# Optimization experiments

Measured on AMD Instinct MI355X. Metric: run time of the kernel, lower is better.

The kernel has to match this reference:

```python
import jax, jax.numpy as jnp
import numpy as np

# Tier config (cumulative d_model [256,1024,2048], cumulative heads [4,12,24], d_k=64)
TIER_OWN = [256, 768, 1024]      # per-tier own hidden dims
HEAD_OUT = [256, 512, 768]       # n_heads_per_tier[i] * d_k
NHS = [4, 8, 12]
DKS = [64, 64, 64]
RANK = 8
IN_OFF = np.cumsum([0] + TIER_OWN)    # [0,256,1024,2048]
OUT_OFF = np.cumsum([0] + HEAD_OUT)   # [0,256,768,1536]


def _block_ut_weight(key, in_dims, out_dims):
    """Full (sum_in, sum_out) matrix with lower-triangular blocks zeroed."""
    io = np.cumsum([0] + list(in_dims))
    oo = np.cumsum([0] + list(out_dims))
    n = len(in_dims)
    mask = np.zeros((io[-1], oo[-1]), dtype=np.float32)
    for i in range(n):
        for j in range(i, n):
            mask[io[i]:io[i + 1], oo[j]:oo[j + 1]] = 1.0
    W = jax.random.normal(key, (io[-1], oo[-1]), dtype=jnp.float32) * 0.02
    return W * jnp.asarray(mask)


def setup_inputs() -> dict:
    key = jax.random.key(0)
    ks = jax.random.split(key, 16)
    B, T, D = 4, 1024, 2048
    x = jax.random.normal(ks[0], (B, T, D), dtype=jnp.float32)
    W_Q = _block_ut_weight(ks[1], TIER_OWN, HEAD_OUT)
    W_K = _block_ut_weight(ks[2], TIER_OWN, HEAD_OUT)
    W_V = _block_ut_weight(ks[3], TIER_OWN, HEAD_OUT)
    W_O = _block_ut_weight(ks[4], HEAD_OUT, TIER_OWN)
    # feedback for tiers 0 and 1 (tier 2 has no higher tiers)
    hi0 = TIER_OWN[1] + TIER_OWN[2]  # 1792
    hi1 = TIER_OWN[2]                # 1024
    FK0 = jax.random.normal(ks[5], (hi0, NHS[0] * RANK), dtype=jnp.float32) * 0.02
    PK0 = jax.random.normal(ks[6], (NHS[0], RANK, DKS[0]), dtype=jnp.float32) * 0.01
    FV0 = jax.random.normal(ks[7], (hi0, NHS[0] * RANK), dtype=jnp.float32) * 0.02
    PV0 = jax.random.normal(ks[8], (NHS[0], RANK, DKS[0]), dtype=jnp.float32) * 0.01
    FK1 = jax.random.normal(ks[9], (hi1, NHS[1] * RANK), dtype=jnp.float32) * 0.02
    PK1 = jax.random.normal(ks[10], (NHS[1], RANK, DKS[1]), dtype=jnp.float32) * 0.01
    FV1 = jax.random.normal(ks[11], (hi1, NHS[1] * RANK), dtype=jnp.float32) * 0.02
    PV1 = jax.random.normal(ks[12], (NHS[1], RANK, DKS[1]), dtype=jnp.float32) * 0.01
    return dict(x=x, W_Q=W_Q, W_K=W_K, W_V=W_V, W_O=W_O,
                FK0=FK0, PK0=PK0, FV0=FV0, PV0=PV0,
                FK1=FK1, PK1=PK1, FV1=FV1, PV1=PV1)


def _forward(x, W_Q, W_K, W_V, W_O, FK0, PK0, FV0, PV0, FK1, PK1, FV1, PV1):
    B, T, _ = x.shape
    Q_all = x @ W_Q
    K_all = x @ W_K
    V_all = x @ W_V
    causal = jnp.tril(jnp.ones((T, T), dtype=bool))
    fb = {0: (FK0, PK0, FV0, PV0), 1: (FK1, PK1, FV1, PV1)}
    head_outs = []
    for tier in range(3):
        nh, dk = NHS[tier], DKS[tier]
        dim = nh * dk
        o = int(OUT_OFF[tier])
        Q = Q_all[..., o:o + dim]
        K = K_all[..., o:o + dim]
        V = V_all[..., o:o + dim]
        if tier in fb:
            Fk, Pk, Fv, Pv = fb[tier]
            h_hi = x[..., int(IN_OFF[tier + 1]):]  # higher tiers' hidden
            c_k = (h_hi @ Fk).reshape(B, T, nh, RANK)
            K = K + jnp.einsum('bthr,hrd->bthd', c_k, Pk).reshape(B, T, dim)
            c_v = (h_hi @ Fv).reshape(B, T, nh, RANK)
            V = V + jnp.einsum('bthr,hrd->bthd', c_v, Pv).reshape(B, T, dim)
        Qh = Q.reshape(B, T, nh, dk).transpose(0, 2, 1, 3)
        Kh = K.reshape(B, T, nh, dk).transpose(0, 2, 1, 3)
        Vh = V.reshape(B, T, nh, dk).transpose(0, 2, 1, 3)
        scores = jnp.einsum('bhqd,bhkd->bhqk', Qh, Kh) / jnp.sqrt(jnp.float32(dk))
        scores = jnp.where(causal, scores, jnp.float32(-1e30))
        attn = jax.nn.softmax(scores, axis=-1)
        out = jnp.einsum('bhqk,bhkd->bhqd', attn, Vh)
        head_outs.append(out.transpose(0, 2, 1, 3).reshape(B, T, dim))
    return jnp.concatenate(head_outs, axis=-1) @ W_O


def reference(x, W_Q, W_K, W_V, W_O, FK0, PK0, FV0, PV0, FK1, PK1, FV1, PV1):
    return _forward(x, W_Q, W_K, W_V, W_O, FK0, PK0, FV0, PV0, FK1, PK1, FV1, PV1)
```

## Files before the change

### kernel.cpp

```cpp
#include <hip/hip_runtime.h>


typedef short bf16x8 __attribute__((ext_vector_type(8)));
typedef float floatx4 __attribute__((ext_vector_type(4)));

__device__ __forceinline__ unsigned short f2bf(float f) {
  unsigned u = __builtin_bit_cast(unsigned, f);
  u += 0x7fffu + ((u >> 16) & 1u);
  return (unsigned short)(u >> 16);
}

__device__ __forceinline__ void gload_lds16(const unsigned short* g, unsigned short* l) {
  __builtin_amdgcn_global_load_lds((const __attribute__((address_space(1))) unsigned int*)g,
                                   (__attribute__((address_space(3))) unsigned int*)l, 16, 0, 0);
}

__global__ __launch_bounds__(256) void k_prep(
    const float* __restrict__ x, unsigned short* __restrict__ X16,
    const float* __restrict__ WQ, const float* __restrict__ WK, const float* __restrict__ WV,
    const float* __restrict__ FK0, const float* __restrict__ PK0,
    const float* __restrict__ FV0, const float* __restrict__ PV0,
    const float* __restrict__ FK1, const float* __restrict__ PK1,
    const float* __restrict__ FV1, const float* __restrict__ PV1,
    unsigned short* __restrict__ WTQKV,
    const float* __restrict__ WO, unsigned short* __restrict__ WTO) {
  __shared__ float tile[32][33];
  __shared__ float Fs[32][9];
  __shared__ float Ps[8][32];
  const int bid = blockIdx.x;
  const int tid = threadIdx.x;
  if (bid < 8192) {
    int i = bid * 256 + tid;
    float4 v = ((const float4*)x)[i];
    union { unsigned short u[4]; uint2 v2; } o;
    o.u[0] = f2bf(v.x); o.u[1] = f2bf(v.y); o.u[2] = f2bf(v.z); o.u[3] = f2bf(v.w);
    ((uint2*)X16)[i] = o.v2;
    return;
  }
  const int tx = tid & 31, ty = tid >> 5;
  if (bid < 17408) {
    int t = bid - 8192;
    int k0 = (t & 63) * 32, n0 = (t >> 6) * 32;
    const float* src; int nboff;
    if (n0 < 1536)      { src = WQ; nboff = n0; }
    else if (n0 < 3072) { src = WK; nboff = n0 - 1536; }
    else                { src = WV; nboff = n0 - 3072; }
#pragma unroll
    for (int j = 0; j < 4; ++j) {
      int kk = ty + j * 8;
      tile[kk][tx] = src[(size_t)(k0 + kk) * 1536 + nboff + tx];
    }
    int corrsel = 0; const float* Fsrc = nullptr; const float* Psrc = nullptr;
    int h = 0, d0 = 0, fs = 0, koff = 0;
    if (n0 >= 1536) {
      bool isK = (n0 < 3072);
      int np0 = isK ? (n0 - 1536) : (n0 - 3072);
      if (np0 < 256) {
        if (k0 >= 256) { corrsel = 1; Fsrc = isK ? FK0 : FV0; Psrc = isK ? PK0 : PV0;
                         h = np0 >> 6; d0 = np0 & 63; fs = 32; koff = k0 - 256; }
      } else if (np0 < 768) {
        if (k0 >= 1024) { corrsel = 1; Fsrc = isK ? FK1 : FV1; Psrc = isK ? PK1 : PV1;
                          h = (np0 - 256) >> 6; d0 = (np0 - 256) & 63; fs = 64; koff = k0 - 1024; }
      }
    }
    if (corrsel) {
      Fs[tid >> 3][tid & 7] = Fsrc[(size_t)(koff + (tid >> 3)) * fs + h * 8 + (tid & 7)];
      Ps[tid >> 5][tid & 31] = Psrc[h * 512 + (tid >> 5) * 64 + d0 + (tid & 31)];
    }
    __syncthreads();
#pragma unroll
    for (int j = 0; j < 4; ++j) {
      int nn = ty + j * 8;
      float v = tile[tx][nn];
      if (corrsel) {
        float c = 0.f;
#pragma unroll
        for (int r = 0; r < 8; ++r) c += Fs[tx][r] * Ps[r][nn];
        v += c;
      }
      WTQKV[(size_t)(n0 + nn) * 2048 + k0 + tx] = f2bf(v);
    }
  } else {
    int t = bid - 17408;
    int k0 = (t % 48) * 32, n0 = (t / 48) * 32;
#pragma unroll
    for (int j = 0; j < 4; ++j)
      tile[ty + j * 8][tx] = WO[(size_t)(k0 + ty + j * 8) * 2048 + n0 + tx];
    __syncthreads();
#pragma unroll
    for (int j = 0; j < 4; ++j)
      WTO[(size_t)(n0 + ty + j * 8) * 1536 + k0 + tx] = f2bf(tile[tx][ty + j * 8]);
  }
}

template <bool OUT_BF16, int MODE>
__global__ __launch_bounds__(256) void k_gemm_bt(const unsigned short* __restrict__ A,
                                                 const unsigned short* __restrict__ Bt,
                                                 void* __restrict__ C, int M, int N, int K) {
  __shared__ unsigned short As[128 * 64];
  __shared__ unsigned short Bs[128 * 64];
  const int tid = threadIdx.x;
  const int wave = tid >> 6, lane = tid & 63;
  const int qd = lane >> 4, ln = lane & 15;
  int idx = blockIdx.x, bx, by;
  if (MODE == 0) {
    if (idx < 960)       { bx = 6 + idx % 30; by = idx / 30; }
    else if (idx < 1088) { int t = idx - 960; bx = 2 + (t & 3); by = t >> 2; }
    else                 { int t = idx - 1088; bx = t & 1; by = t >> 1; }
  } else {
    if (idx < 256)       { bx = 8 + (idx & 7); by = idx >> 3; }
    else if (idx < 448)  { int t = idx - 256; bx = 2 + t % 6; by = t / 6; }
    else                 { int t = idx - 448; bx = t & 1; by = t >> 1; }
  }
  const int bm = by * 128, bn = bx * 128;
  const int wr = wave >> 1, wc = wave & 1;
  int Keff;
  if (MODE == 0) Keff = (bn < 256) ? 256 : (bn < 768 ? 1024 : 2048);
  else           Keff = (bn < 256) ? 256 : (bn < 1024 ? 768 : 1536);
  floatx4 acc[4][4];
#pragma unroll
  for (int i = 0; i < 4; ++i)
#pragma unroll
    for (int j = 0; j < 4; ++j) acc[i][j] = (floatx4){0.f, 0.f, 0.f, 0.f};
  const int rl = lane >> 3;
  const int sg = (lane & 7) ^ rl;
  const unsigned short* gA = A + (size_t)(bm + wave * 32 + rl) * K + sg * 8;
  const unsigned short* gB = Bt + (size_t)(bn + wave * 32 + rl) * K + sg * 8;
  unsigned short* lA = As + wave * 2048;
  unsigned short* lB = Bs + wave * 2048;
  const int l7 = ln & 7;
  for (int k0 = 0; k0 < Keff; k0 += 64) {
    __syncthreads();
#pragma unroll
    for (int i = 0; i < 4; ++i) {
      gload_lds16(gA + (size_t)8 * i * K + k0, lA + i * 512);
      gload_lds16(gB + (size_t)8 * i * K + k0, lB + i * 512);
    }
    __syncthreads();
#pragma unroll
    for (int h = 0; h < 2; ++h) {
      bf16x8 af[4], bfr[4];
#pragma unroll
      for (int mi = 0; mi < 4; ++mi)
        af[mi] = *(const bf16x8*)(As + (wr * 64 + mi * 16 + ln) * 64 + ((h * 4 + qd) ^ l7) * 8);
#pragma unroll
      for (int ni = 0; ni < 4; ++ni)
        bfr[ni] = *(const bf16x8*)(Bs + (wc * 64 + ni * 16 + ln) * 64 + ((h * 4 + qd) ^ l7) * 8);
#pragma unroll
      for (int mi = 0; mi < 4; ++mi)
#pragma unroll
        for (int ni = 0; ni < 4; ++ni)
          acc[mi][ni] = __builtin_amdgcn_mfma_f32_16x16x32_bf16(af[mi], bfr[ni], acc[mi][ni], 0, 0, 0);
    }
  }
#pragma unroll
  for (int mi = 0; mi < 4; ++mi)
#pragma unroll
    for (int r = 0; r < 4; ++r) {
      int row = bm + wr * 64 + mi * 16 + qd * 4 + r;
#pragma unroll
      for (int ni = 0; ni < 4; ++ni) {
        int col = bn + wc * 64 + ni * 16 + ln;
        if (OUT_BF16)
          ((unsigned short*)C)[(size_t)row * N + col] = f2bf(acc[mi][ni][r]);
        else
          ((float*)C)[(size_t)row * N + col] = acc[mi][ni][r];
      }
    }
}

__global__ void k_transpose_v(const unsigned short* __restrict__ QKV,
                              unsigned short* __restrict__ VT) {
  __shared__ unsigned short t[64 * 65];
  const int tt = blockIdx.x * 64, dt = blockIdx.y * 64, b = blockIdx.z;
  const int tid = threadIdx.x;
  const int r = tid >> 3, c0 = (tid & 7) * 8;
#pragma unroll
  for (int i = 0; i < 2; ++i) {
    int tok = r + i * 32;
    union { uint4 v; unsigned short u[8]; } vv;
    vv.v = *(const uint4*)(QKV + (size_t)(b * 1024 + tt + tok) * 4608 + 3072 + dt + c0);
#pragma unroll
    for (int j = 0; j < 8; ++j) t[tok * 65 + c0 + j] = vv.u[j];
  }
  __syncthreads();
#pragma unroll
  for (int i = 0; i < 2; ++i) {
    int d = r + i * 32;
    union { uint4 v; unsigned short u[8]; } vv;
#pragma unroll
    for (int j = 0; j < 8; ++j) vv.u[j] = t[(c0 + j) * 65 + d];
    *(uint4*)(VT + ((size_t)b * 1536 + dt + d) * 1024 + tt + c0) = vv.v;
  }
}

#define LDP 136
__global__ __launch_bounds__(256) void k_attn(const unsigned short* __restrict__ QKV,
                                              const unsigned short* __restrict__ VT,
                                              unsigned short* __restrict__ Oout) {
  __shared__ unsigned short Ks[128 * 64];
  __shared__ unsigned short VTs[64 * 128];
  __shared__ unsigned short Pl[4][16 * LDP];
  const int tid = threadIdx.x;
  const int wave = tid >> 6, lane = tid & 63;
  const int qd = lane >> 4, ln = lane & 15;
  const int qb = (int)gridDim.x - 1 - (int)blockIdx.x;
  const int gh = blockIdx.y, b = blockIdx.z;
  const int T = 1024, LD = 4608;
  const size_t rowbase = (size_t)b * T * LD;
  const int qcol = 64 * gh, kcol = 1536 + 64 * gh;
  const unsigned short* VTg = VT + ((size_t)b * 1536 + 64 * gh) * 1024;
  const float SCALE = 0.18033688f;
  const int q0 = qb * 128 + wave * 16;

  bf16x8 aq[2][2];
#pragma unroll
  for (int j = 0; j < 2; ++j) {
    const unsigned short* qp = QKV + rowbase + (size_t)(q0 + j * 64 + ln) * LD + qcol;
    aq[j][0] = *(const bf16x8*)(qp + qd * 8);
    aq[j][1] = *(const bf16x8*)(qp + 32 + qd * 8);
  }
  floatx4 Oacc[2][4];
#pragma unroll
  for (int j = 0; j < 2; ++j)
#pragma unroll
    for (int i = 0; i < 4; ++i) Oacc[j][i] = (floatx4){0.f, 0.f, 0.f, 0.f};
  float l_lane[2] = {0.f, 0.f};

  const int rk = lane >> 3;
  const int gk = ((lane & 7) ^ rk) * 8;
  const unsigned short* gK = QKV + rowbase + (size_t)(wave * 32 + rk) * LD + kcol + gk;
  unsigned short* lK = Ks + wave * 32 * 64;
  const int rv = lane >> 4;
  const int cv = lane & 15;
  unsigned short* lV = VTs + wave * 16 * 128;
  const unsigned short* gVrow[4];
  int gvcol[4];
#pragma unroll
  for (int i = 0; i < 4; ++i) {
    int d = wave * 16 + 4 * i + rv;
    gVrow[i] = VTg + (size_t)d * 1024;
    gvcol[i] = (cv ^ (4 * i + rv)) * 8;
  }
  const int l7 = ln & 7;

  for (int jt = 0; jt <= qb; ++jt) {
    const int jk = jt * 128;
    const bool diag = (jt == qb);
    __syncthreads();
#pragma unroll
    for (int i = 0; i < 4; ++i) {
      gload_lds16(gK + (size_t)(jk + 8 * i) * LD, lK + i * 512);
      gload_lds16(gVrow[i] + jk + gvcol[i], lV + i * 512);
    }
    __syncthreads();

#pragma unroll
    for (int j = 0; j < 2; ++j) {
      const bool dj0 = diag && (j == 0);
      const int hmax = dj0 ? 4 : 8;
      floatx4 Sc[8];
#pragma unroll
      for (int h = 0; h < 8; ++h) {
        if (h >= hmax) continue;
        Sc[h] = (floatx4){0.f, 0.f, 0.f, 0.f};
        bf16x8 a0 = *(const bf16x8*)(Ks + (h * 16 + ln) * 64 + (qd ^ l7) * 8);
        bf16x8 a1 = *(const bf16x8*)(Ks + (h * 16 + ln) * 64 + ((4 + qd) ^ l7) * 8);
        Sc[h] = __builtin_amdgcn_mfma_f32_16x16x32_bf16(a0, aq[j][0], Sc[h], 0, 0, 0);
        Sc[h] = __builtin_amdgcn_mfma_f32_16x16x32_bf16(a1, aq[j][1], Sc[h], 0, 0, 0);
      }
      const int qrow = q0 + j * 64 + ln;
      unsigned short* pw = Pl[wave];
#pragma unroll
      for (int h = 0; h < 8; ++h) {
        if (h >= hmax) continue;
        union { unsigned short u[4]; uint2 v; } pk;
#pragma unroll
        for (int r = 0; r < 4; ++r) {
          float v = fminf(Sc[h][r] * SCALE, 80.f);
          float p = __builtin_amdgcn_exp2f(v);
          if (diag && (j == 0 || h >= 4)) {
            int key = jk + h * 16 + qd * 4 + r;
            if (key > qrow) p = 0.f;
          }
          l_lane[j] += p;
          pk.u[r] = f2bf(p);
        }
        *(uint2*)(pw + ln * LDP + h * 16 + qd * 4) = pk.v;
      }
      __asm__ volatile("s_waitcnt lgkmcnt(0)" ::: "memory");
      const int smax = dj0 ? 2 : 4;
      bf16x8 pa[4];
#pragma unroll
      for (int s = 0; s < 4; ++s) {
        if (s >= smax) continue;
        pa[s] = *(const bf16x8*)(pw + ln * LDP + s * 32 + qd * 8);
      }
#pragma unroll
      for (int nc = 0; nc < 4; ++nc) {
        const int d = nc * 16 + ln;
#pragma unroll
        for (int s = 0; s < 4; ++s) {
          if (s >= smax) continue;
          bf16x8 bv = *(const bf16x8*)(VTs + d * 128 + (((s * 4 + qd) ^ ln) & 15) * 8);
          Oacc[j][nc] = __builtin_amdgcn_mfma_f32_16x16x32_bf16(pa[s], bv, Oacc[j][nc], 0, 0, 0);
        }
      }
    }
  }
#pragma unroll
  for (int j = 0; j < 2; ++j) {
    float l = l_lane[j];
    l += __shfl_xor(l, 16, 64);
    l += __shfl_xor(l, 32, 64);
#pragma unroll
    for (int r = 0; r < 4; ++r) {
      float inv = 1.0f / __shfl(l, qd * 4 + r, 64);
      size_t row = (size_t)b * T + q0 + j * 64 + qd * 4 + r;
#pragma unroll
      for (int nc = 0; nc < 4; ++nc)
        Oout[row * 1536 + 64 * gh + nc * 16 + ln] = f2bf(Oacc[j][nc][r] * inv);
    }
  }
}

extern "C" void kernel_launch(void* const* d_in, const int* in_sizes, int n_in,
                              void* d_out, int out_size, void* d_ws, size_t ws_size,
                              hipStream_t stream) {
  (void)in_sizes; (void)n_in; (void)out_size; (void)ws_size;
  const float* x   = (const float*)d_in[0];
  const float* WQ  = (const float*)d_in[1];
  const float* WK  = (const float*)d_in[2];
  const float* WV  = (const float*)d_in[3];
  const float* WO  = (const float*)d_in[4];
  const float* FK0 = (const float*)d_in[5];
  const float* PK0 = (const float*)d_in[6];
  const float* FV0 = (const float*)d_in[7];
  const float* PV0 = (const float*)d_in[8];
  const float* FK1 = (const float*)d_in[9];
  const float* PK1 = (const float*)d_in[10];
  const float* FV1 = (const float*)d_in[11];
  const float* PV1 = (const float*)d_in[12];

  char* ws = (char*)d_ws;
  unsigned short* X16   = (unsigned short*)(ws + 0);
  unsigned short* VTb   = X16;
  unsigned short* WTQKV = (unsigned short*)(ws + 16777216);
  unsigned short* QKV   = (unsigned short*)(ws + 35651584);
  unsigned short* ATT   = (unsigned short*)(ws + 73400320);
  unsigned short* WTO   = (unsigned short*)(ws + 85983232);

  k_prep<<<20480, 256, 0, stream>>>(x, X16, WQ, WK, WV,
                                    FK0, PK0, FV0, PV0, FK1, PK1, FV1, PV1,
                                    WTQKV, WO, WTO);
  k_gemm_bt<true, 0><<<1152, 256, 0, stream>>>(X16, WTQKV, QKV, 4096, 4608, 2048);
  k_transpose_v<<<dim3(16, 24, 4), 256, 0, stream>>>(QKV, VTb);
  k_attn<<<dim3(8, 24, 4), 256, 0, stream>>>(QKV, VTb, ATT);
  k_gemm_bt<false, 1><<<512, 256, 0, stream>>>(ATT, WTO, d_out, 4096, 2048, 1536);
}
```

Measured before the change: 323.0 us.

## Replace QKV GEMM with 256x256-tile triple-buffered 512-thread kernel

Adds a dedicated QKV projection GEMM that uses 256x256 output tiles, 8 waves per block, a three-stage LDS ring fed by direct global-to-LDS loads, and an XOR-swizzled LDS layout. It interleaves the A and B prefetch halves with two MFMA phases and raises wave priority around the MFMA work. The block-upper-triangular weight structure is kept by giving each column tile its own effective K length. The goal is more operand reuse per LDS load and better overlap of loads with compute, in exchange for far fewer blocks (288) on a 256-CU part, which risks load imbalance across tiles of different K length.

```diff
diff --git a/kernel.cpp b/kernel.cpp
--- a/kernel.cpp
+++ b/kernel.cpp
@@ -93,6 +93,119 @@
   }
 }
 
+__device__ __forceinline__ int lds_off(int row, int kq) {
+  int L = row >> 1;
+  return L * 64 + ((((row & 1) << 2) | kq) ^ (L & 7)) * 8;
+}
+
+__global__ __launch_bounds__(512) void k_gemm1(const unsigned short* __restrict__ A,
+                                               const unsigned short* __restrict__ Bt,
+                                               unsigned short* __restrict__ C) {
+  __shared__ unsigned short Ls[3][2][8192];
+  const int tid = threadIdx.x;
+  const int wave = tid >> 6, lane = tid & 63;
+  const int qd = lane >> 4, ln = lane & 15;
+  const int wr = wave >> 2, wc = wave & 3;
+  int idx = blockIdx.x, bx, by, Keff;
+  if (idx < 240)      { bx = 3 + idx % 15; by = idx / 15; Keff = 2048; }
+  else if (idx < 272) { int t2 = idx - 240; bx = 1 + (t2 & 1); by = t2 >> 1; Keff = 1024; }
+  else                { bx = 0; by = idx - 272; Keff = 256; }
+  const int bm = by * 256, bn = bx * 256;
+  const int NT = Keff >> 5;
+
+  const int Lr = tid >> 3, sl = tid & 7;
+  const int gg = sl ^ (Lr & 7);
+  const int srow = 2 * Lr + (gg >> 2);
+  const int skg = gg & 3;
+  const unsigned short* gA = A + (size_t)(bm + srow) * 2048 + skg * 8;
+  const unsigned short* gB = Bt + (size_t)(bn + srow) * 2048 + skg * 8;
+
+  int aoff[8], boff[4];
+#pragma unroll
+  for (int mi = 0; mi < 8; ++mi) aoff[mi] = lds_off(wr * 128 + mi * 16 + ln, qd);
+#pragma unroll
+  for (int ni = 0; ni < 4; ++ni) boff[ni] = lds_off(wc * 64 + ni * 16 + ln, qd);
+
+  floatx4 acc[8][4];
+#pragma unroll
+  for (int i = 0; i < 8; ++i)
+#pragma unroll
+    for (int j = 0; j < 4; ++j) acc[i][j] = (floatx4){0.f, 0.f, 0.f, 0.f};
+
+  {
+    unsigned short* d = &Ls[0][0][wave * 512];
+    gload_lds16(gA, d);                 gload_lds16(gA + 128 * 2048, d + 4096);
+    d = &Ls[0][1][wave * 512];
+    gload_lds16(gB, d);                 gload_lds16(gB + 128 * 2048, d + 4096);
+    d = &Ls[1][0][wave * 512];
+    gload_lds16(gA + 32, d);            gload_lds16(gA + 128 * 2048 + 32, d + 4096);
+    d = &Ls[1][1][wave * 512];
+    gload_lds16(gB + 32, d);            gload_lds16(gB + 128 * 2048 + 32, d + 4096);
+  }
+  asm volatile("s_waitcnt vmcnt(4)" ::: "memory");
+  __builtin_amdgcn_s_barrier();
+
+  int b = 0;
+  for (int t = 0; t < NT; ++t) {
+    const int b2 = (b >= 1) ? b - 1 : b + 2;
+    const unsigned short* la = &Ls[b][0][0];
+    const unsigned short* lb = &Ls[b][1][0];
+    const bool pf = (t + 2) < NT;
+    const int k2 = (t + 2) << 5;
+    bf16x8 bfr[4], af[4];
+#pragma unroll
+    for (int ni = 0; ni < 4; ++ni) bfr[ni] = *(const bf16x8*)(lb + boff[ni]);
+#pragma unroll
+    for (int mi = 0; mi < 4; ++mi) af[mi] = *(const bf16x8*)(la + aoff[mi]);
+    if (pf) {
+      unsigned short* d = &Ls[b2][0][wave * 512];
+      gload_lds16(gA + k2, d);
+      gload_lds16(gA + 128 * 2048 + k2, d + 4096);
+    }
+    __builtin_amdgcn_s_barrier();
+    __builtin_amdgcn_s_setprio(1);
+#pragma unroll
+    for (int mi = 0; mi < 4; ++mi)
+#pragma unroll
+      for (int ni = 0; ni < 4; ++ni)
+        acc[mi][ni] = __builtin_amdgcn_mfma_f32_16x16x32_bf16(af[mi], bfr[ni], acc[mi][ni], 0, 0, 0);
+    __builtin_amdgcn_s_setprio(0);
+    __builtin_amdgcn_s_barrier();
+#pragma unroll
+    for (int mi = 0; mi < 4; ++mi) af[mi] = *(const bf16x8*)(la + aoff[4 + mi]);
+    if (pf) {
+      unsigned short* d = &Ls[b2][1][wave * 512];
+      gload_lds16(gB + k2, d);
+      gload_lds16(gB + 128 * 2048 + k2, d + 4096);
+    }
+    __builtin_amdgcn_s_barrier();
+    __builtin_amdgcn_s_setprio(1);
+#pragma unroll
+    for (int mi = 0; mi < 4; ++mi)
+#pragma unroll
+      for (int ni = 0; ni < 4; ++ni)
+        acc[4 + mi][ni] = __builtin_amdgcn_mfma_f32_16x16x32_bf16(af[mi], bfr[ni], acc[4 + mi][ni], 0, 0, 0);
+    __builtin_amdgcn_s_setprio(0);
+    if (t + 1 < NT) {
+      if (pf) asm volatile("s_waitcnt vmcnt(4)" ::: "memory");
+      else    asm volatile("s_waitcnt vmcnt(0)" ::: "memory");
+      __builtin_amdgcn_s_barrier();
+    }
+    b = (b == 2) ? 0 : b + 1;
+  }
+#pragma unroll
+  for (int mi = 0; mi < 8; ++mi)
+#pragma unroll
+    for (int r = 0; r < 4; ++r) {
+      size_t row = (size_t)(bm + wr * 128 + mi * 16 + qd * 4 + r);
+#pragma unroll
+      for (int ni = 0; ni < 4; ++ni) {
+        int col = bn + wc * 64 + ni * 16 + ln;
+        C[row * 4608 + col] = f2bf(acc[mi][ni][r]);
+      }
+    }
+}
+
 template <bool OUT_BF16, int MODE>
 __global__ __launch_bounds__(256) void k_gemm_bt(const unsigned short* __restrict__ A,
                                                  const unsigned short* __restrict__ Bt,
@@ -353,7 +466,7 @@
   k_prep<<<20480, 256, 0, stream>>>(x, X16, WQ, WK, WV,
                                     FK0, PK0, FV0, PV0, FK1, PK1, FV1, PV1,
                                     WTQKV, WO, WTO);
-  k_gemm_bt<true, 0><<<1152, 256, 0, stream>>>(X16, WTQKV, QKV, 4096, 4608, 2048);
+  k_gemm1<<<288, 512, 0, stream>>>(X16, WTQKV, QKV);
   k_transpose_v<<<dim3(16, 24, 4), 256, 0, stream>>>(QKV, VTb);
   k_attn<<<dim3(8, 24, 4), 256, 0, stream>>>(QKV, VTb, ATT);
   k_gemm_bt<false, 1><<<512, 256, 0, stream>>>(ATT, WTO, d_out, 4096, 2048, 1536);
```

New measurement: 333.3 us. 3.2% more time.

## Replace QKV GEMM with 256x256-tile, 4-stage pipelined 512-thread kernel

Applied to the files above, without the earlier changes.

Adds a dedicated QKV projection GEMM. It uses 256x256 output tiles, 8 waves, a 4-buffer LDS pipeline fed by direct global-to-LDS loads with explicit vmcnt waits, XOR-swizzled LDS layout, and s_setprio around the MFMA bursts. Blocks that cover the block-triangular low columns loop over three sub-tiles with shortened K ranges, skipping the zero blocks. The aim is more reuse per tile and better overlap of loads with compute than the old 128x128 GEMM. In exchange it uses 128KB of LDS and high register pressure, which limits occupancy to one block per CU. The grid shrinks to 256 blocks, and the 16 blocks doing the triple sub-tile carry more work, which may cause tail imbalance.

```diff
diff --git a/kernel.cpp b/kernel.cpp
--- a/kernel.cpp
+++ b/kernel.cpp
@@ -93,6 +93,136 @@
   }
 }
 
+__device__ __forceinline__ int lds_off(int row, int kq) {
+  int L = row >> 1;
+  return L * 64 + ((((row & 1) << 2) | kq) ^ (L & 7)) * 8;
+}
+
+#define VM8 asm volatile("s_waitcnt vmcnt(8)" ::: "memory")
+#define VM4 asm volatile("s_waitcnt vmcnt(4)" ::: "memory")
+#define VM0 asm volatile("s_waitcnt vmcnt(0)" ::: "memory")
+#define BAR __builtin_amdgcn_s_barrier()
+
+#define TILE_STEP(AP, BP, AQ, BQ, STG, K3, FIN)                                \
+  do {                                                                         \
+    bf16x8 bfr[4], af[4];                                                      \
+    _Pragma("unroll")                                                          \
+    for (int ni = 0; ni < 4; ++ni) bfr[ni] = *(const bf16x8*)((BP) + boff[ni]);\
+    _Pragma("unroll")                                                          \
+    for (int mi = 0; mi < 4; ++mi) af[mi] = *(const bf16x8*)((AP) + aoff[mi]); \
+    if (STG) {                                                                 \
+      gload_lds16(gA + (K3), (AQ) + wave * 512);                               \
+      gload_lds16(gA + 128 * 2048 + (K3), (AQ) + wave * 512 + 4096);           \
+      gload_lds16(gB + (K3), (BQ) + wave * 512);                               \
+      gload_lds16(gB + 128 * 2048 + (K3), (BQ) + wave * 512 + 4096);           \
+    }                                                                          \
+    BAR;                                                                       \
+    __builtin_amdgcn_s_setprio(1);                                             \
+    _Pragma("unroll")                                                          \
+    for (int mi = 0; mi < 4; ++mi)                                             \
+      _Pragma("unroll")                                                        \
+      for (int ni = 0; ni < 4; ++ni)                                           \
+        acc[mi][ni] = __builtin_amdgcn_mfma_f32_16x16x32_bf16(af[mi], bfr[ni], acc[mi][ni], 0, 0, 0); \
+    __builtin_amdgcn_s_setprio(0);                                             \
+    BAR;                                                                       \
+    _Pragma("unroll")                                                          \
+    for (int mi = 0; mi < 4; ++mi) af[mi] = *(const bf16x8*)((AP) + aoff[4 + mi]); \
+    BAR;                                                                       \
+    __builtin_amdgcn_s_setprio(1);                                             \
+    _Pragma("unroll")                                                          \
+    for (int mi = 0; mi < 4; ++mi)                                             \
+      _Pragma("unroll")                                                        \
+      for (int ni = 0; ni < 4; ++ni)                                           \
+        acc[4 + mi][ni] = __builtin_amdgcn_mfma_f32_16x16x32_bf16(af[mi], bfr[ni], acc[4 + mi][ni], 0, 0, 0); \
+    __builtin_amdgcn_s_setprio(0);                                             \
+    FIN;                                                                       \
+  } while (0)
+
+__global__ __launch_bounds__(512) void k_gemm1(const unsigned short* __restrict__ A,
+                                               const unsigned short* __restrict__ Bt,
+                                               unsigned short* __restrict__ C) {
+  __shared__ unsigned short As0[8192], As1[8192], As2[8192], As3[8192];
+  __shared__ unsigned short Bs0[8192], Bs1[8192], Bs2[8192], Bs3[8192];
+  const int tid = threadIdx.x;
+  const int wave = tid >> 6, lane = tid & 63;
+  const int qd = lane >> 4, ln = lane & 15;
+  const int wr = wave >> 2, wc = wave & 3;
+  const int idx = blockIdx.x;
+  int by, nsub, bns[3], kfs[3];
+  if (idx < 240) {
+    by = idx / 15; nsub = 1;
+    bns[0] = (3 + idx % 15) * 256; kfs[0] = 2048;
+    bns[1] = bns[2] = 0; kfs[1] = kfs[2] = 0;
+  } else {
+    by = idx - 240; nsub = 3;
+    bns[0] = 0;   kfs[0] = 256;
+    bns[1] = 256; kfs[1] = 1024;
+    bns[2] = 512; kfs[2] = 1024;
+  }
+  const int bm = by * 256;
+
+  const int Lr = tid >> 3, sl = tid & 7;
+  const int gg = sl ^ (Lr & 7);
+  const int srow = 2 * Lr + (gg >> 2);
+  const int skg = gg & 3;
+  const unsigned short* gA = A + (size_t)(bm + srow) * 2048 + skg * 8;
+
+  int aoff[8], boff[4];
+#pragma unroll
+  for (int mi = 0; mi < 8; ++mi) aoff[mi] = lds_off(wr * 128 + mi * 16 + ln, qd);
+#pragma unroll
+  for (int ni = 0; ni < 4; ++ni) boff[ni] = lds_off(wc * 64 + ni * 16 + ln, qd);
+
+  for (int s = 0; s < nsub; ++s) {
+    const int bn = bns[s];
+    const int NT = kfs[s] >> 5;
+    const unsigned short* gB = Bt + (size_t)(bn + srow) * 2048 + skg * 8;
+    floatx4 acc[8][4];
+#pragma unroll
+    for (int i = 0; i < 8; ++i)
+#pragma unroll
+      for (int j = 0; j < 4; ++j) acc[i][j] = (floatx4){0.f, 0.f, 0.f, 0.f};
+
+    gload_lds16(gA, As0 + wave * 512);
+    gload_lds16(gA + 128 * 2048, As0 + wave * 512 + 4096);
+    gload_lds16(gB, Bs0 + wave * 512);
+    gload_lds16(gB + 128 * 2048, Bs0 + wave * 512 + 4096);
+    gload_lds16(gA + 32, As1 + wave * 512);
+    gload_lds16(gA + 128 * 2048 + 32, As1 + wave * 512 + 4096);
+    gload_lds16(gB + 32, Bs1 + wave * 512);
+    gload_lds16(gB + 128 * 2048 + 32, Bs1 + wave * 512 + 4096);
+    gload_lds16(gA + 64, As2 + wave * 512);
+    gload_lds16(gA + 128 * 2048 + 64, As2 + wave * 512 + 4096);
+    gload_lds16(gB + 64, Bs2 + wave * 512);
+    gload_lds16(gB + 128 * 2048 + 64, Bs2 + wave * 512 + 4096);
+    VM8;
+    BAR;
+
+    for (int t4 = 0; t4 < NT; t4 += 4) {
+      const bool more = (t4 + 4) < NT;
+      TILE_STEP(As0, Bs0, As3, Bs3, true, (t4 + 3) << 5, VM8; BAR);
+      TILE_STEP(As1, Bs1, As0, Bs0, more, (t4 + 4) << 5,
+                if (more) { VM8; } else { VM4; } BAR);
+      TILE_STEP(As2, Bs2, As1, Bs1, more, (t4 + 5) << 5,
+                if (more) { VM8; } else { VM0; } BAR);
+      TILE_STEP(As3, Bs3, As2, Bs2, more, (t4 + 6) << 5,
+                if (more) { VM8; BAR; });
+    }
+
+#pragma unroll
+    for (int mi = 0; mi < 8; ++mi)
+#pragma unroll
+      for (int r = 0; r < 4; ++r) {
+        size_t row = (size_t)(bm + wr * 128 + mi * 16 + qd * 4 + r);
+#pragma unroll
+        for (int ni = 0; ni < 4; ++ni) {
+          int col = bn + wc * 64 + ni * 16 + ln;
+          C[row * 4608 + col] = f2bf(acc[mi][ni][r]);
+        }
+      }
+  }
+}
+
 template <bool OUT_BF16, int MODE>
 __global__ __launch_bounds__(256) void k_gemm_bt(const unsigned short* __restrict__ A,
                                                  const unsigned short* __restrict__ Bt,
@@ -353,7 +483,7 @@
   k_prep<<<20480, 256, 0, stream>>>(x, X16, WQ, WK, WV,
                                     FK0, PK0, FV0, PV0, FK1, PK1, FV1, PV1,
                                     WTQKV, WO, WTO);
-  k_gemm_bt<true, 0><<<1152, 256, 0, stream>>>(X16, WTQKV, QKV, 4096, 4608, 2048);
+  k_gemm1<<<256, 512, 0, stream>>>(X16, WTQKV, QKV);
   k_transpose_v<<<dim3(16, 24, 4), 256, 0, stream>>>(QKV, VTb);
   k_attn<<<dim3(8, 24, 4), 256, 0, stream>>>(QKV, VTb, ATT);
   k_gemm_bt<false, 1><<<512, 256, 0, stream>>>(ATT, WTO, d_out, 4096, 2048, 1536);
```

Result: slower. 349.3 us (+8.1%).
